# Optimization experiments

Measured on AMD Instinct MI355X. Metric: run time of the kernel, lower is better.

The kernel has to match this reference:

```python
import jax, jax.numpy as jnp
import numpy as np

IN_DIM = 50400
OUT_DIM = 4096
SHARDS = 8
DIM_PER_SHARD = IN_DIM // SHARDS


def setup_inputs() -> dict:
    key = jax.random.key(0)
    k1, k2, k3 = jax.random.split(key, 3)
    x = jax.random.randint(k1, (8, 2048), 0, IN_DIM, dtype=jnp.int64 if jax.config.jax_enable_x64 else jnp.int32)
    # per-shard Linear weights: W[s] is [dim_per_shard, out_dim], TruncatedNormal(1/sqrt(in_dim))
    W = jax.random.normal(k2, (SHARDS, DIM_PER_SHARD, OUT_DIM), dtype=jnp.float32) / np.sqrt(IN_DIM)
    # per-shard Linear bias (haiku default init is zeros; random here to exercise the path)
    b = jax.random.normal(k3, (SHARDS, OUT_DIM), dtype=jnp.float32) * 0.01
    return {"x": x, "W": W, "b": b}


def reference(x, W, b):
    """Math of EmbeddingShard under pmean over 'shard':
    out = (1/S) * sum_s (onehot_s(x) @ W[s] + b[s])
    The one-hot matmul over each vocab shard is exactly a row-gather from the
    concatenated table, so we compute it as a gather (same math, efficient).
    """
    flat_x = x.reshape(-1)                      # [N]
    full_W = W.reshape(IN_Dim := IN_DIM, OUT_DIM)  # [in_dim, out_dim], shards concatenated along vocab
    gathered = jnp.take(full_W, flat_x, axis=0)    # [N, out_dim]
    bias_sum = b.sum(axis=0)                       # sum of per-shard biases
    return (gathered + bias_sum) / SHARDS          # pmean averaging
```

## Files before the change

kernel.cpp:

```cpp
#include <hip/hip_runtime.h>


#define IN_DIM   50400
#define OUT_DIM  4096
#define SHARDS   8
#define N_TOK    16384

#define BLOCKS   2048
#define THREADS  256
#define SLOTS4   (N_TOK * (OUT_DIM / 4))
#define NTHREADS (BLOCKS * THREADS)
#define ITERS    (SLOTS4 / NTHREADS)
#define ROWSTEP  (NTHREADS / (OUT_DIM / 4))

typedef float f4 __attribute__((ext_vector_type(4)));

__global__ __launch_bounds__(256) void bias_sum_kernel(const float* __restrict__ b,
                                                       float* __restrict__ bsum) {
    int j = blockIdx.x * blockDim.x + threadIdx.x;
    if (j < OUT_DIM) {
        float s = 0.0f;
#pragma unroll
        for (int sd = 0; sd < SHARDS; ++sd) s += b[sd * OUT_DIM + j];
        bsum[j] = s * (1.0f / SHARDS);
    }
}

__global__ __launch_bounds__(256) void gather_bias_kernel(const int* __restrict__ x,
                                                          const f4* __restrict__ W4,
                                                          const f4* __restrict__ bsum4,
                                                          f4* __restrict__ out4) {
    const int tid = blockIdx.x * THREADS + threadIdx.x;
    const int j   = tid & (OUT_DIM / 4 - 1);
    const int n0  = tid >> 10;
    const f4 bb = bsum4[j];

#pragma unroll 4
    for (int it = 0; it < ITERS; ++it) {
        const int n   = n0 + it * ROWSTEP;
        const int row = x[n];
        const f4 w = W4[(size_t)row * (OUT_DIM / 4) + j];
        f4 o;
        o.x = fmaf(w.x, 0.125f, bb.x);
        o.y = fmaf(w.y, 0.125f, bb.y);
        o.z = fmaf(w.z, 0.125f, bb.z);
        o.w = fmaf(w.w, 0.125f, bb.w);
        __builtin_nontemporal_store(o, &out4[(size_t)n * (OUT_DIM / 4) + j]);
    }
}

extern "C" void kernel_launch(void* const* d_in, const int* in_sizes, int n_in,
                              void* d_out, int out_size, void* d_ws, size_t ws_size,
                              hipStream_t stream) {
    const int*   x = (const int*)d_in[0];
    const float* W = (const float*)d_in[1];
    const float* b = (const float*)d_in[2];
    float* out  = (float*)d_out;
    float* bsum = (float*)d_ws;

    bias_sum_kernel<<<(OUT_DIM + 255) / 256, 256, 0, stream>>>(b, bsum);
    gather_bias_kernel<<<BLOCKS, THREADS, 0, stream>>>(
        x, (const f4*)W, (const f4*)bsum, (f4*)out);
}
```

Measured before the change: 98.61 us.

## Assign whole output rows per wavefront with scalar row index loads

Restructures the gather so each wavefront owns two full output rows (tokens) and loads each token's index once as a wave-uniform scalar via readfirstlane, then streams the 4096-float row in 16 coalesced steps. Previously every thread reloaded x[n] each iteration and processed scattered rows. This removes the redundant per-iteration index loads and makes the row base addresses scalar. The trade-off is that bias values are now reloaded per iteration instead of held in registers, and there are fewer independent rows in flight per thread.

Result: faster. 96.56 us, median of 2 (-2.1%).

```diff
diff --git a/kernel.cpp b/kernel.cpp
--- a/kernel.cpp
+++ b/kernel.cpp
@@ -8,10 +8,8 @@
 
 #define BLOCKS   2048
 #define THREADS  256
-#define SLOTS4   (N_TOK * (OUT_DIM / 4))
-#define NTHREADS (BLOCKS * THREADS)
-#define ITERS    (SLOTS4 / NTHREADS)
-#define ROWSTEP  (NTHREADS / (OUT_DIM / 4))
+#define NWAVES   (BLOCKS * THREADS / 64)
+#define SLOT4    (OUT_DIM / 4)
 
 typedef float f4 __attribute__((ext_vector_type(4)));
 
@@ -26,26 +24,30 @@
     }
 }
 
-__global__ __launch_bounds__(256) void gather_bias_kernel(const int* __restrict__ x,
+__global__ __launch_bounds__(256) void gather_rows_kernel(const int* __restrict__ x,
                                                           const f4* __restrict__ W4,
                                                           const f4* __restrict__ bsum4,
                                                           f4* __restrict__ out4) {
-    const int tid = blockIdx.x * THREADS + threadIdx.x;
-    const int j   = tid & (OUT_DIM / 4 - 1);
-    const int n0  = tid >> 10;
-    const f4 bb = bsum4[j];
+    const int lane = threadIdx.x & 63;
+    const int wv   = __builtin_amdgcn_readfirstlane((blockIdx.x * THREADS + threadIdx.x) >> 6);
+    const int n0 = wv;
+    const int n1 = wv + NWAVES;
+    const int r0 = x[n0];
+    const int r1 = x[n1];
+
+    const f4* __restrict__ w0 = W4 + (size_t)r0 * SLOT4;
+    const f4* __restrict__ w1 = W4 + (size_t)r1 * SLOT4;
+    f4* __restrict__ o0 = out4 + (size_t)n0 * SLOT4;
+    f4* __restrict__ o1 = out4 + (size_t)n1 * SLOT4;
 
 #pragma unroll 4
-    for (int it = 0; it < ITERS; ++it) {
-        const int n   = n0 + it * ROWSTEP;
-        const int row = x[n];
-        const f4 w = W4[(size_t)row * (OUT_DIM / 4) + j];
-        f4 o;
-        o.x = fmaf(w.x, 0.125f, bb.x);
-        o.y = fmaf(w.y, 0.125f, bb.y);
-        o.z = fmaf(w.z, 0.125f, bb.z);
-        o.w = fmaf(w.w, 0.125f, bb.w);
-        __builtin_nontemporal_store(o, &out4[(size_t)n * (OUT_DIM / 4) + j]);
+    for (int it = 0; it < 16; ++it) {
+        const int j = lane + it * 64;
+        const f4 a  = w0[j];
+        const f4 c  = w1[j];
+        const f4 bb = bsum4[j];
+        __builtin_nontemporal_store(a * 0.125f + bb, &o0[j]);
+        __builtin_nontemporal_store(c * 0.125f + bb, &o1[j]);
     }
 }
 
@@ -58,7 +60,7 @@
     float* out  = (float*)d_out;
     float* bsum = (float*)d_ws;
 
-    bias_sum_kernel<<<(OUT_DIM + 255) / 256, 256, 0, stream>>>(b, bsum);
-    gather_bias_kernel<<<BLOCKS, THREADS, 0, stream>>>(
+    bias_sum_kernel<<<OUT_DIM / 256, 256, 0, stream>>>(b, bsum);
+    gather_rows_kernel<<<BLOCKS, THREADS, 0, stream>>>(
         x, (const f4*)W, (const f4*)bsum, (f4*)out);
 }
```
